# Optimization experiments

Measured on AMD Instinct MI355X. Metric: run time of the kernel, lower is better.

## Reference

```python
import jax, jax.numpy as jnp
import numpy as np

# Model dims (match init_kwargs)
E, D, H, K = 8, 512, 1024, 2   # num_experts, input/output dim, hidden dim, top_k
B, S = 4, 2048                 # batch, seq_len


def setup_inputs() -> dict:
    key = jax.random.key(0)
    ks = jax.random.split(key, 5)
    sd = lambda fan: np.float32(1.0 / np.sqrt(fan))
    return {
        "x": jax.random.normal(ks[0], (B, S, D), jnp.float32),
        "gate_w": jax.random.normal(ks[1], (D, E), jnp.float32) * sd(D),
        "gate_b": jnp.zeros((E,), jnp.float32),
        "w1": jax.random.normal(ks[2], (E, D, H), jnp.float32) * sd(D),
        "b1": jnp.zeros((E, H), jnp.float32),
        "w2": jax.random.normal(ks[3], (E, H, D), jnp.float32) * sd(H),
        "b2": jnp.zeros((E, D), jnp.float32),
    }


def reference(x, gate_w, gate_b, w1, b1, w2, b2):
    # x: [B, S, D]
    Bb, Ss, Dd = x.shape
    xf = x.reshape(-1, Dd)                              # [N, D], N = B*S

    # Router: softmax over experts, top-k, renormalize selected weights
    logits = xf @ gate_w + gate_b                        # [N, E]
    probs = jax.nn.softmax(logits, axis=-1)              # [N, E]
    top_w, top_i = jax.lax.top_k(probs, K)               # [N, K]
    top_w = top_w / top_w.sum(axis=-1, keepdims=True)

    # Per-token combine weight for each expert (0 if not routed).
    onehot = jax.nn.one_hot(top_i, E, dtype=probs.dtype)  # [N, K, E]
    combine = jnp.einsum("nke,nk->ne", onehot, top_w)     # [N, E]

    # Expert MLPs. Dropout is inactive at inference (identity).
    # h: [E, N, H]; GELU exact (torch nn.GELU default uses erf)
    h = jax.nn.gelu(jnp.einsum("nd,edh->enh", xf, w1) + b1[:, None, :],
                    approximate=False)
    y = jnp.einsum("enh,ehd->end", h, w2) + b2[:, None, :]  # [E, N, D]

    # Weighted combine: tokens not routed to expert e have combine[:, e] == 0.
    out = jnp.einsum("end,ne->nd", y, combine).reshape(Bb, Ss, Dd)
    return out, probs.reshape(Bb, Ss, E)
```

## Files before the change

kernel.cpp:

```cpp
#include <hip/hip_runtime.h>
#include <stdint.h>

#define N_TOK 8192
#define DIM   512
#define HID   1024
#define NE    8
#define NSLOT 16384
#define MAXSLOT 17408

typedef __attribute__((ext_vector_type(8))) short short8;
typedef __attribute__((ext_vector_type(4))) float f32x4;

#define W1T_OFF  0ull
#define W2T_OFF  8388608ull
#define H_OFF    16777216ull
#define Y_OFF    52428800ull
#define XBF_OFF  52428800ull
#define TOPI_OFF 70254592ull
#define TOPW_OFF 70320128ull
#define SLOT_OFF 70385664ull
#define ROWS_OFF 70451200ull
#define RW_OFF   70520832ull
#define CNT_OFF  70590464ull

__device__ __forceinline__ unsigned int f2bfu(float f) {
  union { float f; unsigned int i; } v; v.f = f;
  unsigned int u = v.i;
  return (u + 0x7FFFu + ((u >> 16) & 1u)) >> 16;
}
__device__ __forceinline__ float bf2f(unsigned int u) {
  union { unsigned int i; float f; } v; v.i = (u & 0xFFFFu) << 16; return v.f;
}
__device__ __forceinline__ void async16(void* lds, const void* g) {
  __builtin_amdgcn_global_load_lds(
      (const __attribute__((address_space(1))) unsigned int*)g,
      (__attribute__((address_space(3))) unsigned int*)lds, 16, 0, 0);
}

__global__ __launch_bounds__(256) void k_transpose(
    const float* __restrict__ w1, const float* __restrict__ w2,
    unsigned short* __restrict__ w1t, unsigned short* __restrict__ w2t) {
  __shared__ unsigned short tile[64][68];
  int b = blockIdx.x, tid = threadIdx.x;
  const float* src; unsigned short* dst; int R, C;
  if (b < 1024) { int e = b >> 7; int t = b & 127;
    src = w1 + (size_t)e * 524288; dst = w1t + (size_t)e * 524288; R = 512; C = 1024;
    int tr = t >> 4, tc = t & 15;
    src += (size_t)tr * 64 * C + tc * 64; dst += (size_t)tc * 64 * R + tr * 64;
  } else { b -= 1024; int e = b >> 7; int t = b & 127;
    src = w2 + (size_t)e * 524288; dst = w2t + (size_t)e * 524288; R = 1024; C = 512;
    int tr = t >> 3, tc = t & 7;
    src += (size_t)tr * 64 * C + tc * 64; dst += (size_t)tc * 64 * R + tr * 64;
  }
#pragma unroll
  for (int i = 0; i < 4; ++i) {
    int l = i * 256 + tid;
    int r = l >> 4, c4 = (l & 15) << 2;
    float4 v = *(const float4*)(src + (size_t)r * C + c4);
    tile[r][c4 + 0] = (unsigned short)f2bfu(v.x);
    tile[r][c4 + 1] = (unsigned short)f2bfu(v.y);
    tile[r][c4 + 2] = (unsigned short)f2bfu(v.z);
    tile[r][c4 + 3] = (unsigned short)f2bfu(v.w);
  }
  __syncthreads();
#pragma unroll
  for (int i = 0; i < 4; ++i) {
    int l = i * 256 + tid;
    int rr = l >> 4, c4 = (l & 15) << 2;
    ushort4 v;
    v.x = tile[c4 + 0][rr]; v.y = tile[c4 + 1][rr]; v.z = tile[c4 + 2][rr]; v.w = tile[c4 + 3][rr];
    *(ushort4*)(dst + (size_t)rr * R + c4) = v;
  }
}

__global__ __launch_bounds__(256) void k_router(
    const float* __restrict__ x, const float* __restrict__ gw,
    const float* __restrict__ gb, float* __restrict__ probs_out,
    int2* __restrict__ topi, float2* __restrict__ topw,
    unsigned short* __restrict__ xbf) {
  int wave = threadIdx.x >> 6, lane = threadIdx.x & 63;
  int n = blockIdx.x * 4 + wave;
  const float4* xr = (const float4*)(x + (size_t)n * DIM);
  float4 x0 = xr[lane * 2], x1 = xr[lane * 2 + 1];
  float xf[8] = {x0.x, x0.y, x0.z, x0.w, x1.x, x1.y, x1.z, x1.w};
  uint4 pa;
  pa.x = f2bfu(xf[0]) | (f2bfu(xf[1]) << 16);
  pa.y = f2bfu(xf[2]) | (f2bfu(xf[3]) << 16);
  pa.z = f2bfu(xf[4]) | (f2bfu(xf[5]) << 16);
  pa.w = f2bfu(xf[6]) | (f2bfu(xf[7]) << 16);
  *(uint4*)(xbf + (size_t)n * DIM + lane * 8) = pa;
  float acc[8] = {0.f,0.f,0.f,0.f,0.f,0.f,0.f,0.f};
  const float4* gwr = (const float4*)gw;
#pragma unroll
  for (int j = 0; j < 8; ++j) {
    int d = lane * 8 + j;
    float4 g0 = gwr[d * 2], g1 = gwr[d * 2 + 1];
    acc[0] += xf[j] * g0.x; acc[1] += xf[j] * g0.y; acc[2] += xf[j] * g0.z; acc[3] += xf[j] * g0.w;
    acc[4] += xf[j] * g1.x; acc[5] += xf[j] * g1.y; acc[6] += xf[j] * g1.z; acc[7] += xf[j] * g1.w;
  }
#pragma unroll
  for (int o = 1; o < 64; o <<= 1)
#pragma unroll
    for (int e = 0; e < 8; ++e) acc[e] += __shfl_xor(acc[e], o, 64);
  float p[8], mx = -1e30f, s = 0.f;
#pragma unroll
  for (int e = 0; e < 8; ++e) { p[e] = acc[e] + gb[e]; mx = fmaxf(mx, p[e]); }
#pragma unroll
  for (int e = 0; e < 8; ++e) { p[e] = __expf(p[e] - mx); s += p[e]; }
  float inv = 1.f / s;
#pragma unroll
  for (int e = 0; e < 8; ++e) p[e] *= inv;
  if (lane < 8) probs_out[(size_t)n * NE + lane] = p[lane];
  if (lane == 0) {
    int i0 = 0; float v0 = p[0];
#pragma unroll
    for (int e = 1; e < 8; ++e) if (p[e] > v0) { v0 = p[e]; i0 = e; }
    int i1 = -1; float v1 = -1.f;
#pragma unroll
    for (int e = 0; e < 8; ++e) if (e != i0 && p[e] > v1) { v1 = p[e]; i1 = e; }
    float sw = 1.f / (v0 + v1);
    topi[n] = make_int2(i0, i1);
    topw[n] = make_float2(v0 * sw, v1 * sw);
  }
}

__global__ __launch_bounds__(1024) void k_count(
    const int2* __restrict__ topi, int* __restrict__ meta, int* __restrict__ chunk_base,
    int* __restrict__ rows, float* __restrict__ rw) {
  __shared__ int ch[32][8];
  __shared__ int tot[8], poff_s[9], tiles_s[8];
  int t = threadIdx.x;
  int g = t >> 5;
  if (t < 256) ((int*)ch)[t] = 0;
  __syncthreads();
  int c[8] = {0,0,0,0,0,0,0,0};
  int base_tok = t * 8;
#pragma unroll
  for (int i = 0; i < 8; ++i) {
    int2 e = topi[base_tok + i];
#pragma unroll
    for (int k = 0; k < 8; ++k) c[k] += (e.x == k) + (e.y == k);
  }
#pragma unroll
  for (int k = 0; k < 8; ++k) if (c[k]) atomicAdd(&ch[g][k], c[k]);
  __syncthreads();
  if (t < 8) {
    int a = 0;
#pragma unroll
    for (int b = 0; b < 32; ++b) { int v = ch[b][t]; ch[b][t] = a; a += v; }
    tot[t] = a; meta[t] = a;
  }
  __syncthreads();
  if (t == 0) {
    int a = 0, ts = 0;
#pragma unroll
    for (int e = 0; e < 8; ++e) {
      int tiles = (tot[e] + 127) >> 7;
      poff_s[e] = a; tiles_s[e] = tiles;
      meta[16 + e] = a; meta[32 + e] = ts;
      a += tiles << 7; ts += tiles;
    }
    poff_s[8] = a; meta[24] = a; meta[40] = ts;
  }
  __syncthreads();
  if (t < 256) {
    int b = t >> 3, e = t & 7;
    chunk_base[t] = poff_s[e] + ch[b][e];
  }
#pragma unroll
  for (int e = 0; e < 8; ++e) {
    int padn = (tiles_s[e] << 7) - tot[e];
    if (t < padn) {
      int s = poff_s[e] + tot[e] + t;
      rows[s] = 0; rw[s] = 0.f;
    }
  }
}

__global__ __launch_bounds__(256) void k_assign(
    const int2* __restrict__ topi, const float2* __restrict__ topw,
    const int* __restrict__ chunk_base,
    int* __restrict__ rows, float* __restrict__ rw, int* __restrict__ slot_of) {
  __shared__ int lcnt[8];
  __shared__ int lbase[8];
  int t = threadIdx.x, b = blockIdx.x;
  if (t < 8) { lcnt[t] = 0; lbase[t] = chunk_base[b * 8 + t]; }
  __syncthreads();
  int n = b * 256 + t;
  int2 ei = topi[n]; float2 wv = topw[n];
  int r0 = atomicAdd(&lcnt[ei.x], 1);
  int r1 = atomicAdd(&lcnt[ei.y], 1);
  int s0 = lbase[ei.x] + r0;
  int s1 = lbase[ei.y] + r1;
  rows[s0] = n; rw[s0] = wv.x; slot_of[2 * n] = s0;
  rows[s1] = n; rw[s1] = wv.y; slot_of[2 * n + 1] = s1;
}

__global__ __launch_bounds__(256) void k_gemm1(
    const unsigned short* __restrict__ xbf, const unsigned short* __restrict__ w1t,
    const float* __restrict__ b1, const int* __restrict__ meta,
    const int* __restrict__ rows, unsigned short* __restrict__ h) {
  int t = blockIdx.x;
  if (t >= meta[40]) return;
  int e = 0;
#pragma unroll
  for (int i = 1; i < 8; ++i) if (t >= meta[32 + i]) e = i;
  int mt = t - meta[32 + e];
  int row0 = meta[16 + e] + (mt << 7);
  int nt = blockIdx.y;
  __shared__ __align__(16) unsigned short As[128 * 64];
  __shared__ __align__(16) unsigned short Bs[128 * 64];
  __shared__ int rows_l[128];
  int tid = threadIdx.x;
  if (tid < 128) rows_l[tid] = rows[row0 + tid];
  __syncthreads();
  int wave = tid >> 6, lane = tid & 63;
  int wr = wave & 1, wc = wave >> 1;
  f32x4 acc[4][4] = {};
  const unsigned short* bBase = w1t + (size_t)e * HID * DIM + (size_t)(nt * 128) * DIM;

  for (int k0 = 0; k0 < DIM; k0 += 64) {
#pragma unroll
    for (int j = 0; j < 4; ++j) {
      int s = j * 256 + tid;
      int r = s >> 3;
      int cg = ((s & 7) ^ (r & 7)) << 3;
      async16(&As[(j * 256 + wave * 64) * 8], xbf + (size_t)rows_l[r] * DIM + k0 + cg);
      async16(&Bs[(j * 256 + wave * 64) * 8], bBase + (size_t)r * DIM + k0 + cg);
    }
    __syncthreads();
#pragma unroll
    for (int kk = 0; kk < 2; ++kk) {
      int ca = kk * 4 + (lane >> 4);
      short8 a[4], b[4];
#pragma unroll
      for (int m = 0; m < 4; ++m) {
        int ra = wr * 64 + m * 16 + (lane & 15);
        a[m] = *(const short8*)&As[(ra * 8 + (ca ^ (ra & 7))) * 8];
      }
#pragma unroll
      for (int nb = 0; nb < 4; ++nb) {
        int rb = wc * 64 + nb * 16 + (lane & 15);
        b[nb] = *(const short8*)&Bs[(rb * 8 + (ca ^ (rb & 7))) * 8];
      }
#pragma unroll
      for (int m = 0; m < 4; ++m)
#pragma unroll
        for (int nb = 0; nb < 4; ++nb)
          acc[m][nb] = __builtin_amdgcn_mfma_f32_16x16x32_bf16(a[m], b[nb], acc[m][nb], 0, 0, 0);
    }
    __syncthreads();
  }
  int rq = (lane >> 4) * 4;
#pragma unroll
  for (int m = 0; m < 4; ++m) {
    int rl = wr * 64 + m * 16 + rq;
#pragma unroll
    for (int nb = 0; nb < 4; ++nb) {
      int col = nt * 128 + wc * 64 + nb * 16 + (lane & 15);
      float bias = b1[e * HID + col];
#pragma unroll
      for (int i = 0; i < 4; ++i) {
        float v = acc[m][nb][i] + bias;
        float g = 0.5f * v * (1.0f + erff(v * 0.70710678118654752f));
        h[(size_t)(row0 + rl + i) * HID + col] = (unsigned short)f2bfu(g);
      }
    }
  }
}

__global__ __launch_bounds__(256) void k_gemm2(
    const unsigned short* __restrict__ h, const unsigned short* __restrict__ w2t,
    const float* __restrict__ b2, const int* __restrict__ meta,
    const float* __restrict__ rw, unsigned short* __restrict__ y) {
  int t = blockIdx.x;
  if (t >= meta[40]) return;
  int e = 0;
#pragma unroll
  for (int i = 1; i < 8; ++i) if (t >= meta[32 + i]) e = i;
  int mt = t - meta[32 + e];
  int row0 = meta[16 + e] + (mt << 7);
  int nt = blockIdx.y;
  __shared__ __align__(16) unsigned short As[128 * 64];
  __shared__ __align__(16) unsigned short Bs[128 * 64];
  int tid = threadIdx.x;
  int wave = tid >> 6, lane = tid & 63;
  int wr = wave & 1, wc = wave >> 1;
  f32x4 acc[4][4] = {};
  const unsigned short* aBase = h + (size_t)row0 * HID;
  const unsigned short* bBase = w2t + (size_t)e * DIM * HID + (size_t)(nt * 128) * HID;

  for (int k0 = 0; k0 < HID; k0 += 64) {
#pragma unroll
    for (int j = 0; j < 4; ++j) {
      int s = j * 256 + tid;
      int r = s >> 3;
      int cg = ((s & 7) ^ (r & 7)) << 3;
      async16(&As[(j * 256 + wave * 64) * 8], aBase + (size_t)r * HID + k0 + cg);
      async16(&Bs[(j * 256 + wave * 64) * 8], bBase + (size_t)r * HID + k0 + cg);
    }
    __syncthreads();
#pragma unroll
    for (int kk = 0; kk < 2; ++kk) {
      int ca = kk * 4 + (lane >> 4);
      short8 a[4], b[4];
#pragma unroll
      for (int m = 0; m < 4; ++m) {
        int ra = wr * 64 + m * 16 + (lane & 15);
        a[m] = *(const short8*)&As[(ra * 8 + (ca ^ (ra & 7))) * 8];
      }
#pragma unroll
      for (int nb = 0; nb < 4; ++nb) {
        int rb = wc * 64 + nb * 16 + (lane & 15);
        b[nb] = *(const short8*)&Bs[(rb * 8 + (ca ^ (rb & 7))) * 8];
      }
#pragma unroll
      for (int m = 0; m < 4; ++m)
#pragma unroll
        for (int nb = 0; nb < 4; ++nb)
          acc[m][nb] = __builtin_amdgcn_mfma_f32_16x16x32_bf16(a[m], b[nb], acc[m][nb], 0, 0, 0);
    }
    __syncthreads();
  }
  int rq = (lane >> 4) * 4;
#pragma unroll
  for (int m = 0; m < 4; ++m) {
    int rl = wr * 64 + m * 16 + rq;
#pragma unroll
    for (int nb = 0; nb < 4; ++nb) {
      int col = nt * 128 + wc * 64 + nb * 16 + (lane & 15);
      float bias = b2[e * DIM + col];
#pragma unroll
      for (int i = 0; i < 4; ++i) {
        int rsl = row0 + rl + i;
        float w = rw[rsl];
        y[(size_t)rsl * DIM + col] = (unsigned short)f2bfu((acc[m][nb][i] + bias) * w);
      }
    }
  }
}

__global__ __launch_bounds__(256) void k_combine(
    const unsigned short* __restrict__ y, const int* __restrict__ slot_of,
    float* __restrict__ out) {
  int t = blockIdx.x * 256 + threadIdx.x;
  int n = t >> 6, c = (t & 63) << 3;
  int s0 = slot_of[2 * n], s1 = slot_of[2 * n + 1];
  uint4 u0 = *(const uint4*)(y + (size_t)s0 * DIM + c);
  uint4 u1 = *(const uint4*)(y + (size_t)s1 * DIM + c);
  float4 o0, o1;
  o0.x = bf2f(u0.x) + bf2f(u1.x); o0.y = bf2f(u0.x >> 16) + bf2f(u1.x >> 16);
  o0.z = bf2f(u0.y) + bf2f(u1.y); o0.w = bf2f(u0.y >> 16) + bf2f(u1.y >> 16);
  o1.x = bf2f(u0.z) + bf2f(u1.z); o1.y = bf2f(u0.z >> 16) + bf2f(u1.z >> 16);
  o1.z = bf2f(u0.w) + bf2f(u1.w); o1.w = bf2f(u0.w >> 16) + bf2f(u1.w >> 16);
  *(float4*)(out + (size_t)n * DIM + c) = o0;
  *(float4*)(out + (size_t)n * DIM + c + 4) = o1;
}

extern "C" void kernel_launch(void* const* d_in, const int* in_sizes, int n_in,
                              void* d_out, int out_size, void* d_ws, size_t ws_size,
                              hipStream_t stream) {
  const float* x  = (const float*)d_in[0];
  const float* gw = (const float*)d_in[1];
  const float* gb = (const float*)d_in[2];
  const float* w1 = (const float*)d_in[3];
  const float* b1 = (const float*)d_in[4];
  const float* w2 = (const float*)d_in[5];
  const float* b2 = (const float*)d_in[6];
  float* out = (float*)d_out;
  char* ws = (char*)d_ws;

  unsigned short* w1t = (unsigned short*)(ws + W1T_OFF);
  unsigned short* w2t = (unsigned short*)(ws + W2T_OFF);
  unsigned short* h   = (unsigned short*)(ws + H_OFF);
  unsigned short* y   = (unsigned short*)(ws + Y_OFF);
  unsigned short* xbf = (unsigned short*)(ws + XBF_OFF);
  int2*   topi    = (int2*)(ws + TOPI_OFF);
  float2* topw    = (float2*)(ws + TOPW_OFF);
  int*    slot_of = (int*)(ws + SLOT_OFF);
  int*    rows    = (int*)(ws + ROWS_OFF);
  float*  rw      = (float*)(ws + RW_OFF);
  int*    meta    = (int*)(ws + CNT_OFF);
  int*    chunk_base = meta + 64;
  float*  probs   = out + (size_t)N_TOK * DIM;

  k_transpose<<<dim3(2048), dim3(256), 0, stream>>>(w1, w2, w1t, w2t);
  k_router   <<<dim3(2048), dim3(256), 0, stream>>>(x, gw, gb, probs, topi, topw, xbf);
  k_count    <<<dim3(1),    dim3(1024), 0, stream>>>(topi, meta, chunk_base, rows, rw);
  k_assign   <<<dim3(32),   dim3(256), 0, stream>>>(topi, topw, chunk_base, rows, rw, slot_of);
  k_gemm1    <<<dim3(136, 8), dim3(256), 0, stream>>>(xbf, w1t, b1, meta, rows, h);
  k_gemm2    <<<dim3(136, 4), dim3(256), 0, stream>>>(h, w2t, b2, meta, rw, y);
  k_combine  <<<dim3(2048), dim3(256), 0, stream>>>(y, slot_of, out);
}
```

Baseline: 240.0 us.

## Swap MFMA operands for row-contiguous epilogue stores, hoist load addresses, fast GELU

```diff
diff --git a/kernel.cpp b/kernel.cpp
--- a/kernel.cpp
+++ b/kernel.cpp
@@ -30,6 +30,12 @@
 }
 __device__ __forceinline__ float bf2f(unsigned int u) {
   union { unsigned int i; float f; } v; v.i = (u & 0xFFFFu) << 16; return v.f;
+}
+__device__ __forceinline__ float gelu_f(float x) {
+  float x2 = x * x;
+  float u = x * (1.59576912f + 0.07135481f * x2);
+  float ez = __expf(-u);
+  return x * __builtin_amdgcn_rcpf(1.0f + ez);
 }
 __device__ __forceinline__ void async16(void* lds, const void* g) {
   __builtin_amdgcn_global_load_lds(
@@ -219,52 +225,63 @@
   f32x4 acc[4][4] = {};
   const unsigned short* bBase = w1t + (size_t)e * HID * DIM + (size_t)(nt * 128) * DIM;
 
+  const unsigned short* ga[4]; const unsigned short* gb[4];
+#pragma unroll
+  for (int j = 0; j < 4; ++j) {
+    int s = j * 256 + tid;
+    int r = s >> 3;
+    int cg = ((s & 7) ^ (r & 7)) << 3;
+    ga[j] = xbf + (size_t)rows_l[r] * DIM + cg;
+    gb[j] = bBase + (size_t)r * DIM + cg;
+  }
+
   for (int k0 = 0; k0 < DIM; k0 += 64) {
 #pragma unroll
     for (int j = 0; j < 4; ++j) {
-      int s = j * 256 + tid;
-      int r = s >> 3;
-      int cg = ((s & 7) ^ (r & 7)) << 3;
-      async16(&As[(j * 256 + wave * 64) * 8], xbf + (size_t)rows_l[r] * DIM + k0 + cg);
-      async16(&Bs[(j * 256 + wave * 64) * 8], bBase + (size_t)r * DIM + k0 + cg);
+      async16(&As[(j * 256 + wave * 64) * 8], ga[j] + k0);
+      async16(&Bs[(j * 256 + wave * 64) * 8], gb[j] + k0);
     }
     __syncthreads();
 #pragma unroll
     for (int kk = 0; kk < 2; ++kk) {
       int ca = kk * 4 + (lane >> 4);
-      short8 a[4], b[4];
-#pragma unroll
-      for (int m = 0; m < 4; ++m) {
-        int ra = wr * 64 + m * 16 + (lane & 15);
-        a[m] = *(const short8*)&As[(ra * 8 + (ca ^ (ra & 7))) * 8];
+      short8 tf[4], wf[4];
+#pragma unroll
+      for (int am = 0; am < 4; ++am) {
+        int ra = wr * 64 + am * 16 + (lane & 15);
+        tf[am] = *(const short8*)&As[(ra * 8 + (ca ^ (ra & 7))) * 8];
       }
 #pragma unroll
-      for (int nb = 0; nb < 4; ++nb) {
-        int rb = wc * 64 + nb * 16 + (lane & 15);
-        b[nb] = *(const short8*)&Bs[(rb * 8 + (ca ^ (rb & 7))) * 8];
+      for (int an = 0; an < 4; ++an) {
+        int rb = wc * 64 + an * 16 + (lane & 15);
+        wf[an] = *(const short8*)&Bs[(rb * 8 + (ca ^ (rb & 7))) * 8];
       }
 #pragma unroll
-      for (int m = 0; m < 4; ++m)
-#pragma unroll
-        for (int nb = 0; nb < 4; ++nb)
-          acc[m][nb] = __builtin_amdgcn_mfma_f32_16x16x32_bf16(a[m], b[nb], acc[m][nb], 0, 0, 0);
+      for (int an = 0; an < 4; ++an)
+#pragma unroll
+        for (int am = 0; am < 4; ++am)
+          acc[an][am] = __builtin_amdgcn_mfma_f32_16x16x32_bf16(wf[an], tf[am], acc[an][am], 0, 0, 0);
     }
     __syncthreads();
   }
-  int rq = (lane >> 4) * 4;
-#pragma unroll
-  for (int m = 0; m < 4; ++m) {
-    int rl = wr * 64 + m * 16 + rq;
-#pragma unroll
-    for (int nb = 0; nb < 4; ++nb) {
-      int col = nt * 128 + wc * 64 + nb * 16 + (lane & 15);
-      float bias = b1[e * HID + col];
-#pragma unroll
-      for (int i = 0; i < 4; ++i) {
-        float v = acc[m][nb][i] + bias;
-        float g = 0.5f * v * (1.0f + erff(v * 0.70710678118654752f));
-        h[(size_t)(row0 + rl + i) * HID + col] = (unsigned short)f2bfu(g);
-      }
+  int ml = lane & 15, q = lane >> 4;
+#pragma unroll
+  for (int am = 0; am < 4; ++am) {
+    int slot_r = row0 + wr * 64 + am * 16 + ml;
+    unsigned short* hrow = h + (size_t)slot_r * HID;
+#pragma unroll
+    for (int an = 0; an < 4; ++an) {
+      int colb = nt * 128 + wc * 64 + an * 16 + q * 4;
+      float4 bias = *(const float4*)&b1[e * HID + colb];
+      f32x4 v = acc[an][am];
+      float g0 = gelu_f(v[0] + bias.x);
+      float g1 = gelu_f(v[1] + bias.y);
+      float g2 = gelu_f(v[2] + bias.z);
+      float g3 = gelu_f(v[3] + bias.w);
+      uint2 pk;
+      pk.x = f2bfu(g0) | (f2bfu(g1) << 16);
+      pk.y = f2bfu(g2) | (f2bfu(g3) << 16);
+      *(uint2*)(hrow + colb) = pk;
     }
   }
 }
@@ -290,52 +307,60 @@
   const unsigned short* aBase = h + (size_t)row0 * HID;
   const unsigned short* bBase = w2t + (size_t)e * DIM * HID + (size_t)(nt * 128) * HID;
 
+  const unsigned short* ga[4]; const unsigned short* gb[4];
+#pragma unroll
+  for (int j = 0; j < 4; ++j) {
+    int s = j * 256 + tid;
+    int r = s >> 3;
+    int cg = ((s & 7) ^ (r & 7)) << 3;
+    ga[j] = aBase + (size_t)r * HID + cg;
+    gb[j] = bBase + (size_t)r * HID + cg;
+  }
+
   for (int k0 = 0; k0 < HID; k0 += 64) {
 #pragma unroll
     for (int j = 0; j < 4; ++j) {
-      int s = j * 256 + tid;
-      int r = s >> 3;
-      int cg = ((s & 7) ^ (r & 7)) << 3;
-      async16(&As[(j * 256 + wave * 64) * 8], aBase + (size_t)r * HID + k0 + cg);
-      async16(&Bs[(j * 256 + wave * 64) * 8], bBase + (size_t)r * HID + k0 + cg);
+      async16(&As[(j * 256 + wave * 64) * 8], ga[j] + k0);
+      async16(&Bs[(j * 256 + wave * 64) * 8], gb[j] + k0);
     }
     __syncthreads();
 #pragma unroll
     for (int kk = 0; kk < 2; ++kk) {
       int ca = kk * 4 + (lane >> 4);
-      short8 a[4], b[4];
-#pragma unroll
-      for (int m = 0; m < 4; ++m) {
-        int ra = wr * 64 + m * 16 + (lane & 15);
-        a[m] = *(const short8*)&As[(ra * 8 + (ca ^ (ra & 7))) * 8];
+      short8 tf[4], wf[4];
+#pragma unroll
+      for (int am = 0; am < 4; ++am) {
+        int ra = wr * 64 + am * 16 + (lane & 15);
+        tf[am] = *(const short8*)&As[(ra * 8 + (ca ^ (ra & 7))) * 8];
       }
 #pragma unroll
-      for (int nb = 0; nb < 4; ++nb) {
-        int rb = wc * 64 + nb * 16 + (lane & 15);
-        b[nb] = *(const short8*)&Bs[(rb * 8 + (ca ^ (rb & 7))) * 8];
+      for (int an = 0; an < 4; ++an) {
+        int rb = wc * 64 + an * 16 + (lane & 15);
+        wf[an] = *(const short8*)&Bs[(rb * 8 + (ca ^ (rb & 7))) * 8];
       }
 #pragma unroll
-      for (int m = 0; m < 4; ++m)
-#pragma unroll
-        for (int nb = 0; nb < 4; ++nb)
-          acc[m][nb] = __builtin_amdgcn_mfma_f32_16x16x32_bf16(a[m], b[nb], acc[m][nb], 0, 0, 0);
+      for (int an = 0; an < 4; ++an)
+#pragma unroll
+        for (int am = 0; am < 4; ++am)
+          acc[an][am] = __builtin_amdgcn_mfma_f32_16x16x32_bf16(wf[an], tf[am], acc[an][am], 0, 0, 0);
     }
     __syncthreads();
   }
-  int rq = (lane >> 4) * 4;
-#pragma unroll
-  for (int m = 0; m < 4; ++m) {
-    int rl = wr * 64 + m * 16 + rq;
-#pragma unroll
-    for (int nb = 0; nb < 4; ++nb) {
-      int col = nt * 128 + wc * 64 + nb * 16 + (lane & 15);
-      float bias = b2[e * DIM + col];
-#pragma unroll
-      for (int i = 0; i < 4; ++i) {
-        int rsl = row0 + rl + i;
-        float w = rw[rsl];
-        y[(size_t)rsl * DIM + col] = (unsigned short)f2bfu((acc[m][nb][i] + bias) * w);
-      }
+  int ml = lane & 15, q = lane >> 4;
+#pragma unroll
+  for (int am = 0; am < 4; ++am) {
+    int slot_r = row0 + wr * 64 + am * 16 + ml;
+    float w = rw[slot_r];
+    unsigned short* yrow = y + (size_t)slot_r * DIM;
+#pragma unroll
+    for (int an = 0; an < 4; ++an) {
+      int colb = nt * 128 + wc * 64 + an * 16 + q * 4;
+      float4 bias = *(const float4*)&b2[e * DIM + colb];
+      f32x4 v = acc[an][am];
+      uint2 pk;
+      pk.x = f2bfu((v[0] + bias.x) * w) | (f2bfu((v[1] + bias.y) * w) << 16);
+      pk.y = f2bfu((v[2] + bias.z) * w) | (f2bfu((v[3] + bias.w) * w) << 16);
+      *(uint2*)(yrow + colb) = pk;
     }
   }
 }
```

Result: faster. 214.3 us (-10.7%).
